# Optimization experiments

Hardware: AMD Instinct MI355X
Metric: run time of the kernel (lower is better)

## Reference

```python
import jax, jax.numpy as jnp
import numpy as np


def setup_inputs() -> dict:
    key = jax.random.key(0)
    ks = jax.random.split(key, 12)
    B, Nq, Ns, NODES = 128, 16, 256, 3
    V, E, C, H, OUT, NA = 50000, 300, 1024, 8, 300, 5000
    s = 0.05
    return {
        "he_ques": jax.random.randint(ks[0], (B, Nq, NODES), 0, V),
        "he_kg": jax.random.randint(ks[1], (B, Ns, NODES), 0, V),
        "emb": jax.random.normal(ks[2], (V, E), jnp.float32) * s,
        "q2h_w": jax.random.normal(ks[3], (C, E * NODES), jnp.float32) * s,
        "q2h_b": jax.random.normal(ks[4], (C,), jnp.float32) * s,
        "k2h_w": jax.random.normal(ks[5], (C, E * NODES), jnp.float32) * s,
        "k2h_b": jax.random.normal(ks[6], (C,), jnp.float32) * s,
        "h2att_w": jax.random.normal(ks[7], (H, C), jnp.float32) * s,
        "h2att_b": jax.random.normal(ks[8], (H,), jnp.float32) * s,
        "fc_w": jax.random.normal(ks[9], (OUT, C * H), jnp.float32) * s,
        "fc_b": jax.random.normal(ks[10], (OUT,), jnp.float32) * s,
        "glove_cands": jax.random.normal(ks[11], (NA, OUT), jnp.float32) * s,
    }


def reference(he_ques, he_kg, emb, q2h_w, q2h_b, k2h_w, k2h_b,
              h2att_w, h2att_b, fc_w, fc_b, glove_cands):
    B, Nq, _ = he_ques.shape
    Ns = he_kg.shape[1]
    H, C = h2att_w.shape
    # embed node indices and flatten per-hyperedge: [B, N, nodes*E]
    hq = emb[he_ques].reshape(B, Nq, -1)
    hs = emb[he_kg].reshape(B, Ns, -1)
    # linear projections (dropout p=0 in eval)
    hq = hq @ q2h_w.T + q2h_b  # [B, Nq, C]
    hs = hs @ k2h_w.T + k2h_b  # [B, Ns, C]
    # bilinear attention logits: h2att(outer(hq, hs)) fused into one einsum
    # logits[b,h,q,s] = sum_c hq[b,q,c] * hs[b,s,c] * W[h,c] + b[h]
    logits = jnp.einsum('bqc,bsc,hc->bhqs', hq, hs, h2att_w) + h2att_b[None, :, None, None]
    att = jax.nn.softmax(logits.reshape(B, H, Nq * Ns), axis=2).reshape(B, H, Nq, Ns)
    # per-head bilinear readout (replaces the per-head repeat+matmul loop):
    # out[b,h,c] = sum_{q,s} hq[b,q,c] * att[b,h,q,s] * hs[b,s,c]
    pooled = jnp.einsum('bqc,bhqs,bsc->bhc', hq, att, hs).reshape(B, H * C)
    out = pooled @ fc_w.T + fc_b  # [B, n_out]
    sim = out @ glove_cands.T  # [B, n_ans]
    return jax.nn.log_softmax(sim, axis=1)
```

## Files before the change

### kernel.cpp

```cpp
#include <hip/hip_runtime.h>
#include <stdint.h>


typedef short s16x8 __attribute__((ext_vector_type(8)));
typedef float f32x4 __attribute__((ext_vector_type(4)));

#define ASYNC_CP16(gsrc, ldst)                                                  \
  __builtin_amdgcn_global_load_lds(                                             \
      (const __attribute__((address_space(1))) void*)(gsrc),                    \
      (__attribute__((address_space(3))) void*)(ldst), 16, 0, 0)

__device__ __forceinline__ float bfr2f(uint16_t u) {
  return __builtin_bit_cast(float, (uint32_t)u << 16);
}
__device__ __forceinline__ uint16_t f2bfr(float f) {
  uint32_t u = __builtin_bit_cast(uint32_t, f);
  u += 0x7fffu + ((u >> 16) & 1u);
  return (uint16_t)(u >> 16);
}

__global__ __launch_bounds__(256) void cvt_all(
    const float* __restrict__ emb_f, const float* __restrict__ wk_f,
    const float* __restrict__ wq_f, const float* __restrict__ glove_f,
    const float* __restrict__ watt_f, const float* __restrict__ fc_f,
    uint16_t* __restrict__ EMB, uint16_t* __restrict__ WK,
    uint16_t* __restrict__ WQ, uint16_t* __restrict__ GLV,
    uint16_t* __restrict__ WATT, uint16_t* __restrict__ WFC) {
  const int idx = blockIdx.x * 256 + threadIdx.x;
  const int TOT1 = 61264 * 80;
  const int TOT2 = TOT1 + 1024;
  if (idx < TOT1) {
    const int row = idx / 80, j = idx % 80;
    const float* src;
    uint16_t* dst;
    int srow, svalid;
    if (row < 50000) {
      src = emb_f; dst = EMB; srow = row; svalid = 1;
    } else if (row < 53072) {
      src = wk_f; dst = WK; srow = row - 50000; svalid = 1;
    } else if (row < 56144) {
      src = wq_f; dst = WQ; srow = row - 53072; svalid = 1;
    } else {
      src = glove_f; dst = GLV; srow = row - 56144; svalid = (srow < 5000);
    }
    float4 v = make_float4(0.f, 0.f, 0.f, 0.f);
    if (svalid && j < 75) v = *(const float4*)(src + (size_t)srow * 300 + j * 4);
    ushort4 o;
    o.x = f2bfr(v.x); o.y = f2bfr(v.y); o.z = f2bfr(v.z); o.w = f2bfr(v.w);
    *(ushort4*)(dst + (size_t)srow * 320 + j * 4) = o;
  } else if (idx < TOT2) {
    const int i = idx - TOT1;
    float4 a = *(const float4*)(watt_f + i * 8);
    float4 b = *(const float4*)(watt_f + i * 8 + 4);
    ushort4 o0, o1;
    o0.x = f2bfr(a.x); o0.y = f2bfr(a.y); o0.z = f2bfr(a.z); o0.w = f2bfr(a.w);
    o1.x = f2bfr(b.x); o1.y = f2bfr(b.y); o1.z = f2bfr(b.z); o1.w = f2bfr(b.w);
    *(ushort4*)(WATT + i * 8) = o0;
    *(ushort4*)(WATT + i * 8 + 4) = o1;
  } else {
    const int i4 = idx - TOT2;
    if (i4 < 384 * 2048) {
      const int pos = i4 * 4;
      const int r = pos >> 13, c = pos & 8191;
      float4 v = make_float4(0.f, 0.f, 0.f, 0.f);
      if (r < 300) v = *(const float4*)(fc_f + (size_t)r * 8192 + c);
      ushort4 o;
      o.x = f2bfr(v.x); o.y = f2bfr(v.y); o.z = f2bfr(v.z); o.w = f2bfr(v.w);
      *(ushort4*)(WFC + (size_t)r * 8192 + c) = o;
    }
  }
}

__global__ __launch_bounds__(256) void gemm_gather2(
    const int* __restrict__ heK, const int* __restrict__ heQ,
    const uint16_t* __restrict__ emb,
    const uint16_t* __restrict__ WKp, const uint16_t* __restrict__ WQp,
    const float* __restrict__ bK, const float* __restrict__ bQ,
    uint16_t* __restrict__ HS, uint16_t* __restrict__ HQ) {
  __shared__ uint16_t ring[2 * 8192];
  __shared__ int sIdx[384];
  char* ringB = (char*)ring;

  const int t = threadIdx.x;
  const int lane = t & 63, wave = t >> 6;
  const int wr = wave >> 1, wc = wave & 1;
  const int fr = lane & 15, fq = lane >> 4;
  const int srow = t >> 2, skg = t & 3;
  const int skg2 = skg ^ ((srow >> 1) & 3);

  const int v = blockIdx.x + 8 * blockIdx.y;
  const int w = (v & 7) * 272 + (v >> 3);
  const int bx = w & 7, by = w >> 3;
  const int n0 = bx * 128;
  const bool isK = by < 256;
  const int m0 = (isK ? by : by - 256) * 128;
  const int* he = isK ? heK : heQ;
  const uint16_t* W = isK ? WKp : WQp;
  const float* bias = isK ? bK : bQ;
  uint16_t* C = isK ? HS : HQ;

  for (int i = t; i < 384; i += 256) sIdx[i] = he[(long)m0 * 3 + i];
  __syncthreads();

  uint32_t ea[2][3];
#pragma unroll
  for (int h = 0; h < 2; h++)
#pragma unroll
    for (int nd = 0; nd < 3; nd++)
      ea[h][nd] =
          (uint32_t)sIdx[(h * 64 + srow) * 3 + nd] * 640u + (uint32_t)(skg2 * 16);
  const uint16_t* Wr0 = W + (long)(n0 + srow) * 960 + skg2 * 8;
  const uint16_t* Wr1 = W + (long)(n0 + 64 + srow) * 960 + skg2 * 8;

  f32x4 zv = {0.f, 0.f, 0.f, 0.f};
  f32x4 acc[4][4];
#pragma unroll
  for (int i = 0; i < 4; i++)
#pragma unroll
    for (int j = 0; j < 4; j++) acc[i][j] = zv;

  int snd = 0, skk = 0, sk = 0, sbuf = 0;
  auto STAGE = [&]() {
    const int bb = sbuf * 16384;
    const uint32_t e0 = snd == 0 ? ea[0][0] : (snd == 1 ? ea[0][1] : ea[0][2]);
    const uint32_t e1 = snd == 0 ? ea[1][0] : (snd == 1 ? ea[1][1] : ea[1][2]);
    ASYNC_CP16((const char*)emb + e0 + skk * 64, ringB + bb + t * 16);
    ASYNC_CP16((const char*)emb + e1 + skk * 64, ringB + bb + 4096 + t * 16);
    ASYNC_CP16(Wr0 + sk, ringB + bb + 8192 + t * 16);
    ASYNC_CP16(Wr1 + sk, ringB + bb + 12288 + t * 16);
    sk += 32;
    if (++skk == 10) { skk = 0; ++snd; }
    sbuf ^= 1;
  };

  STAGE();

  const int fsw = (fq ^ ((fr >> 1) & 3)) * 8;
  int aof[4], bof[4];
#pragma unroll
  for (int mi = 0; mi < 4; mi++) aof[mi] = (wr * 64 + mi * 16 + fr) * 32 + fsw;
#pragma unroll
  for (int ni = 0; ni < 4; ni++)
    bof[ni] = 4096 + (wc * 64 + ni * 16 + fr) * 32 + fsw;

  int cbuf = 0;
  for (int kt = 0; kt < 30; ++kt) {
    if (kt < 29) {
      STAGE();
      asm volatile("s_waitcnt vmcnt(4)" ::: "memory");
    } else {
      asm volatile("s_waitcnt vmcnt(0)" ::: "memory");
    }
    __builtin_amdgcn_s_barrier();
    asm volatile("" ::: "memory");
    const uint16_t* base = ring + cbuf * 8192;
    s16x8 af[4], bv[4];
#pragma unroll
    for (int mi = 0; mi < 4; mi++) af[mi] = *(const s16x8*)(base + aof[mi]);
#pragma unroll
    for (int ni = 0; ni < 4; ni++) bv[ni] = *(const s16x8*)(base + bof[ni]);
    __builtin_amdgcn_s_setprio(1);
#pragma unroll
    for (int mi = 0; mi < 4; mi++)
#pragma unroll
      for (int ni = 0; ni < 4; ni++)
        acc[mi][ni] = __builtin_amdgcn_mfma_f32_16x16x32_bf16(
            af[mi], bv[ni], acc[mi][ni], 0, 0, 0);
    __builtin_amdgcn_s_setprio(0);
    asm volatile("s_waitcnt lgkmcnt(0)" ::: "memory");
    __builtin_amdgcn_s_barrier();
    cbuf ^= 1;
  }

#pragma unroll
  for (int ni = 0; ni < 4; ni++) {
    const int gn = n0 + wc * 64 + ni * 16 + fr;
    const float bval = bias[gn];
#pragma unroll
    for (int mi = 0; mi < 4; mi++) {
      const int gmb = m0 + wr * 64 + mi * 16 + fq * 4;
      uint16_t* cp = C + (long)gmb * 1024 + gn;
      cp[0]    = f2bfr(acc[mi][ni][0] + bval);
      cp[1024] = f2bfr(acc[mi][ni][1] + bval);
      cp[2048] = f2bfr(acc[mi][ni][2] + bval);
      cp[3072] = f2bfr(acc[mi][ni][3] + bval);
    }
  }
}

__global__ __launch_bounds__(256) void gemm_logits(
    const uint16_t* __restrict__ hq, const uint16_t* __restrict__ watt,
    const uint16_t* __restrict__ hs, uint16_t* __restrict__ att) {
  __shared__ uint16_t ring[3 * 4096];
  char* ringB = (char*)ring;

  const int t = threadIdx.x;
  const int lane = t & 63, wave = t >> 6;
  const int wr = wave >> 1, wc = wave & 1;
  const int fr = lane & 15, fq = lane >> 4;
  const int srow = t >> 2, skg = t & 3;
  const int skg2 = skg ^ ((srow >> 1) & 3);

  int bx = blockIdx.x, bz = blockIdx.z;
  {
    const int v = bx + 2 * bz;
    const int w = (v & 7) * 32 + (v >> 3);
    bx = w & 1;
    bz = w >> 1;
  }
  const int n0 = bx * 128;

  const uint16_t* Bs0 = hs + (long)bz * 262144 + (long)(n0 + srow) * 1024 + skg2 * 8;
  const uint16_t* Bs1 = hs + (long)bz * 262144 + (long)(n0 + 64 + srow) * 1024 + skg2 * 8;
  const uint16_t* hqp = hq + (long)(bz * 16 + fr) * 1024 + fq * 8;
  const uint16_t* wp0 = watt + (long)(wr * 4 + 0) * 1024 + fq * 8;
  const uint16_t* wp1 = watt + (long)(wr * 4 + 1) * 1024 + fq * 8;
  const uint16_t* wp2 = watt + (long)(wr * 4 + 2) * 1024 + fq * 8;
  const uint16_t* wp3 = watt + (long)(wr * 4 + 3) * 1024 + fq * 8;

  f32x4 zv = {0.f, 0.f, 0.f, 0.f};
  f32x4 acc[4][4];
#pragma unroll
  for (int i = 0; i < 4; i++)
#pragma unroll
    for (int j = 0; j < 4; j++) acc[i][j] = zv;

  int sbuf = 0, cbuf = 0;
  ASYNC_CP16(Bs0, ringB + t * 16);
  ASYNC_CP16(Bs1, ringB + 2048 + t * 16);
  ASYNC_CP16(Bs0 + 32, ringB + 4096 + t * 16);
  ASYNC_CP16(Bs1 + 32, ringB + 4096 + 2048 + t * 16);
  sbuf = 2;
  s16x8 hqA = *(const s16x8*)(hqp);
  s16x8 wA0 = *(const s16x8*)(wp0), wA1 = *(const s16x8*)(wp1);
  s16x8 wA2 = *(const s16x8*)(wp2), wA3 = *(const s16x8*)(wp3);
  s16x8 hqB, wB0, wB1, wB2, wB3;

  const int fsw = (fq ^ ((fr >> 1) & 3)) * 8;
  int bof[4];
#pragma unroll
  for (int ni = 0; ni < 4; ni++)
    bof[ni] = (wc * 64 + ni * 16 + fr) * 32 + fsw;

#define LOG_BODY(KT, HQS, W0S, W1S, W2S, W3S, HQD, W0D, W1D, W2D, W3D)          \
  {                                                                             \
    const int kt = (KT);                                                        \
    if (kt + 2 < 32) {                                                          \
      ASYNC_CP16(Bs0 + (kt + 2) * 32, ringB + sbuf * 4096 + t * 16);            \
      ASYNC_CP16(Bs1 + (kt + 2) * 32, ringB + sbuf * 4096 + 2048 + t * 16);     \
      if (++sbuf == 3) sbuf = 0;                                                \
    }                                                                           \
    if (kt + 1 < 32) {                                                          \
      const int ko = (kt + 1) * 32;                                             \
      HQD = *(const s16x8*)(hqp + ko);                                          \
      W0D = *(const s16x8*)(wp0 + ko); W1D = *(const s16x8*)(wp1 + ko);         \
      W2D = *(const s16x8*)(wp2 + ko); W3D = *(const s16x8*)(wp3 + ko);         \
    }                                                                           \
    asm volatile("s_waitcnt vmcnt(7)" ::: "memory");                            \
    __builtin_amdgcn_s_barrier();                                               \
    asm volatile("" ::: "memory");                                              \
    s16x8 af0, af1, af2, af3, bv[4];                                            \
    _Pragma("unroll") for (int j = 0; j < 8; j++) {                             \
      const float hv = bfr2f((uint16_t)HQS[j]);                                 \
      af0[j] = (short)f2bfr(hv * bfr2f((uint16_t)W0S[j]));                      \
      af1[j] = (short)f2bfr(hv * bfr2f((uint16_t)W1S[j]));                      \
      af2[j] = (short)f2bfr(hv * bfr2f((uint16_t)W2S[j]));                      \
      af3[j] = (short)f2bfr(hv * bfr2f((uint16_t)W3S[j]));                      \
    }                                                                           \
    const uint16_t* base = ring + cbuf * 4096;                                  \
    _Pragma("unroll") for (int ni = 0; ni < 4; ni++)                            \
        bv[ni] = *(const s16x8*)(base + bof[ni]);                               \
    __builtin_amdgcn_s_setprio(1);                                              \
    _Pragma("unroll") for (int ni = 0; ni < 4; ni++) {                          \
      acc[0][ni] = __builtin_amdgcn_mfma_f32_16x16x32_bf16(af0, bv[ni],         \
                                                           acc[0][ni], 0, 0, 0);\
      acc[1][ni] = __builtin_amdgcn_mfma_f32_16x16x32_bf16(af1, bv[ni],         \
                                                           acc[1][ni], 0, 0, 0);\
      acc[2][ni] = __builtin_amdgcn_mfma_f32_16x16x32_bf16(af2, bv[ni],         \
                                                           acc[2][ni], 0, 0, 0);\
      acc[3][ni] = __builtin_amdgcn_mfma_f32_16x16x32_bf16(af3, bv[ni],         \
                                                           acc[3][ni], 0, 0, 0);\
    }                                                                           \
    __builtin_amdgcn_s_setprio(0);                                              \
    asm volatile("s_waitcnt lgkmcnt(0)" ::: "memory");                          \
    __builtin_amdgcn_s_barrier();                                               \
    if (++cbuf == 3) cbuf = 0;                                                  \
  }

  for (int kt2 = 0; kt2 < 32; kt2 += 2) {
    LOG_BODY(kt2, hqA, wA0, wA1, wA2, wA3, hqB, wB0, wB1, wB2, wB3);
    LOG_BODY(kt2 + 1, hqB, wB0, wB1, wB2, wB3, hqA, wA0, wA1, wA2, wA3);
  }
#undef LOG_BODY

#pragma unroll
  for (int ni = 0; ni < 4; ni++) {
    const int gn = n0 + wc * 64 + ni * 16 + fr;
#pragma unroll
    for (int mi = 0; mi < 4; mi++)
#pragma unroll
      for (int j = 0; j < 4; j++) {
        const int gm = wr * 64 + mi * 16 + fq * 4 + j;
        att[(long)bz * 32768 + gm * 256 + gn] = f2bfr(acc[mi][ni][j]);
      }
  }
}

template <int SWZ>
__global__ __launch_bounds__(256) void gemm_pipe(
    const uint16_t* __restrict__ A, int lda, long sAb,
    const uint16_t* __restrict__ Bt, int ldb, long sBb,
    int ksteps, int kchunk,
    float* __restrict__ Cf, int ldcf, int nmax, long sCf) {
  __shared__ uint16_t ring[3 * 8192];
  char* ringB = (char*)ring;

  const int t = threadIdx.x;
  const int lane = t & 63, wave = t >> 6;
  const int wr = wave >> 1, wc = wave & 1;
  const int fr = lane & 15, fq = lane >> 4;
  const int srow = t >> 2, skg = t & 3;
  const int skg2 = skg ^ ((srow >> 1) & 3);

  int bx = blockIdx.x, bz = blockIdx.z;
  if (SWZ) {
    const int nwg = gridDim.x * gridDim.z;
    const int v = bx + gridDim.x * bz;
    const int w = (v & 7) * (nwg >> 3) + (v >> 3);
    bx = w % gridDim.x;
    bz = w / gridDim.x;
  }
  const int m0 = blockIdx.y * 128, n0 = bx * 128;
  const uint16_t* Ab = A + (long)bz * sAb;
  const uint16_t* Bb = Bt;

  f32x4 zv = {0.f, 0.f, 0.f, 0.f};
  f32x4 acc[4][4];
#pragma unroll
  for (int i = 0; i < 4; i++)
#pragma unroll
    for (int j = 0; j < 4; j++) acc[i][j] = zv;

  const long kbase = (long)bz * kchunk;
  const uint16_t* As0 = Ab + (long)(m0 + srow) * lda + kbase + skg2 * 8;
  const uint16_t* As1 = Ab + (long)(m0 + 64 + srow) * lda + kbase + skg2 * 8;
  const uint16_t* Bs0 = Bb + (long)(n0 + srow) * ldb + kbase + skg2 * 8;
  const uint16_t* Bs1 = Bb + (long)(n0 + 64 + srow) * ldb + kbase + skg2 * 8;

  int sk = 0, sbuf = 0;
  auto STAGE = [&]() {
    const int bb = sbuf * 16384;
    ASYNC_CP16(As0 + sk, ringB + bb + t * 16);
    ASYNC_CP16(As1 + sk, ringB + bb + 4096 + t * 16);
    ASYNC_CP16(Bs0 + sk, ringB + bb + 8192 + t * 16);
    ASYNC_CP16(Bs1 + sk, ringB + bb + 12288 + t * 16);
    sk += 32;
    if (++sbuf == 3) sbuf = 0;
  };

  STAGE();
  STAGE();

  const int fsw = (fq ^ ((fr >> 1) & 3)) * 8;
  int aof[4], bof[4];
#pragma unroll
  for (int mi = 0; mi < 4; mi++) aof[mi] = (wr * 64 + mi * 16 + fr) * 32 + fsw;
#pragma unroll
  for (int ni = 0; ni < 4; ni++)
    bof[ni] = 4096 + (wc * 64 + ni * 16 + fr) * 32 + fsw;

  int cbuf = 0;
  for (int kt = 0; kt < ksteps; ++kt) {
    if (kt + 2 < ksteps) STAGE();
    if (kt + 2 < ksteps)      asm volatile("s_waitcnt vmcnt(8)" ::: "memory");
    else if (kt + 1 < ksteps) asm volatile("s_waitcnt vmcnt(4)" ::: "memory");
    else                      asm volatile("s_waitcnt vmcnt(0)" ::: "memory");
    __builtin_amdgcn_s_barrier();
    asm volatile("" ::: "memory");
    const uint16_t* base = ring + cbuf * 8192;
    s16x8 af[4], bv[4];
#pragma unroll
    for (int mi = 0; mi < 4; mi++) af[mi] = *(const s16x8*)(base + aof[mi]);
#pragma unroll
    for (int ni = 0; ni < 4; ni++) bv[ni] = *(const s16x8*)(base + bof[ni]);
#pragma unroll
    for (int mi = 0; mi < 4; mi++)
#pragma unroll
      for (int ni = 0; ni < 4; ni++)
        acc[mi][ni] = __builtin_amdgcn_mfma_f32_16x16x32_bf16(
            af[mi], bv[ni], acc[mi][ni], 0, 0, 0);
    asm volatile("s_waitcnt lgkmcnt(0)" ::: "memory");
    __builtin_amdgcn_s_barrier();
    if (++cbuf == 3) cbuf = 0;
  }

#pragma unroll
  for (int ni = 0; ni < 4; ni++) {
    const int gn = n0 + wc * 64 + ni * 16 + fr;
    if (gn < nmax) {
#pragma unroll
      for (int mi = 0; mi < 4; mi++)
#pragma unroll
        for (int j = 0; j < 4; j++) {
          const int gm = m0 + wr * 64 + mi * 16 + fq * 4 + j;
          Cf[(long)bz * sCf + (long)gm * ldcf + gn] = acc[mi][ni][j];
        }
    }
  }
}

__global__ __launch_bounds__(256) void gemm_pv(
    const uint16_t* __restrict__ att, const uint16_t* __restrict__ hs,
    const uint16_t* __restrict__ hqp, uint16_t* __restrict__ pooled) {
  __shared__ uint16_t sT[128 * 264];
  __shared__ uint16_t sA[4096];
  __shared__ uint16_t sHq[2048];

  const int t = threadIdx.x;
  const int lane = t & 63, wave = t >> 6;
  const int wr = wave >> 1, wc = wave & 1;
  const int fr = lane & 15, fq = lane >> 4;
  const int srow = t >> 2, skg = t & 3;
  const int skg2 = skg ^ ((srow >> 1) & 3);

  int bx = blockIdx.x, bz = blockIdx.z;
  {
    const int v = bx + 8 * bz;
    const int w = (v & 7) * 128 + (v >> 3);
    bx = w & 7;
    bz = w >> 3;
  }
  const int n0 = bx * 128;

  const uint16_t* hsb = hs + (long)bz * 262144;
  const int sloc = t & 15, c8 = t >> 4;
  s16x8 vv[16];
#pragma unroll
  for (int p = 0; p < 16; p++)
    vv[p] = *(const s16x8*)(hsb + (long)(p * 16 + sloc) * 1024 + n0 + c8 * 8);
  *(s16x8*)(sHq + (t >> 4) * 128 + (t & 15) * 8) =
      *(const s16x8*)(hqp + (long)bz * 16384 + (long)(t >> 4) * 1024 + n0 +
                      (t & 15) * 8);
#pragma unroll
  for (int p = 0; p < 16; p++) {
    const int s = p * 16 + sloc;
#pragma unroll
    for (int j = 0; j < 8; j++)
      sT[(c8 * 8 + j) * 264 + s] = (uint16_t)vv[p][j];
  }
  __syncthreads();

  f32x4 zv = {0.f, 0.f, 0.f, 0.f};
  f32x4 acc[4][4];
#pragma unroll
  for (int i = 0; i < 4; i++)
#pragma unroll
    for (int j = 0; j < 4; j++) acc[i][j] = zv;

  const uint16_t* As0 = att + (long)bz * 32768 + (long)srow * 256 + skg2 * 8;
  const uint16_t* As1 = att + (long)bz * 32768 + (long)(64 + srow) * 256 + skg2 * 8;

  const int fsw = (fq ^ ((fr >> 1) & 3)) * 8;
  int aof[4];
#pragma unroll
  for (int mi = 0; mi < 4; mi++) aof[mi] = (wr * 64 + mi * 16 + fr) * 32 + fsw;

  for (int kt = 0; kt < 8; ++kt) {
    ASYNC_CP16(As0 + kt * 32, (char*)sA + t * 16);
    ASYNC_CP16(As1 + kt * 32, (char*)sA + 4096 + t * 16);
    __syncthreads();
    s16x8 af[4], bv[4];
#pragma unroll
    for (int mi = 0; mi < 4; mi++) af[mi] = *(const s16x8*)(sA + aof[mi]);
#pragma unroll
    for (int ni = 0; ni < 4; ni++)
      bv[ni] = *(const s16x8*)(sT + (wc * 64 + ni * 16 + fr) * 264 + kt * 32 +
                               fq * 8);
    __builtin_amdgcn_s_setprio(1);
#pragma unroll
    for (int mi = 0; mi < 4; mi++)
#pragma unroll
      for (int ni = 0; ni < 4; ni++)
        acc[mi][ni] = __builtin_amdgcn_mfma_f32_16x16x32_bf16(
            af[mi], bv[ni], acc[mi][ni], 0, 0, 0);
    __builtin_amdgcn_s_setprio(0);
    __syncthreads();
  }

#pragma unroll
  for (int mi = 0; mi < 4; mi++) {
    const int hh = wr * 4 + mi;
#pragma unroll
    for (int ni = 0; ni < 4; ni++) {
      const int col = wc * 64 + ni * 16 + fr;
      float p = 0.f;
#pragma unroll
      for (int j = 0; j < 4; j++)
        p += acc[mi][ni][j] * bfr2f(sHq[(fq * 4 + j) * 128 + col]);
      p += __shfl_xor(p, 16);
      p += __shfl_xor(p, 32);
      if (fq == 0)
        pooled[(long)bz * 8192 + hh * 1024 + n0 + col] = f2bfr(p);
    }
  }
}

__global__ __launch_bounds__(256) void softmax_att(uint16_t* __restrict__ att) {
  const int b = blockIdx.x >> 3, h = blockIdx.x & 7;
  uint16_t* base = att + (long)b * 32768 + h * 4096;
  const int t = threadIdx.x;
  __shared__ float red[8];
  s16x8 v0 = *(const s16x8*)(base + t * 16);
  s16x8 v1 = *(const s16x8*)(base + t * 16 + 8);
  float f[16];
#pragma unroll
  for (int j = 0; j < 8; j++) {
    f[j] = bfr2f((uint16_t)v0[j]);
    f[8 + j] = bfr2f((uint16_t)v1[j]);
  }
  float mx = f[0];
#pragma unroll
  for (int j = 1; j < 16; j++) mx = fmaxf(mx, f[j]);
#pragma unroll
  for (int d = 1; d < 64; d <<= 1) mx = fmaxf(mx, __shfl_xor(mx, d));
  if ((t & 63) == 0) red[t >> 6] = mx;
  __syncthreads();
  mx = fmaxf(fmaxf(red[0], red[1]), fmaxf(red[2], red[3]));
  float s = 0.f;
#pragma unroll
  for (int j = 0; j < 16; j++) {
    f[j] = __expf(f[j] - mx);
    s += f[j];
  }
#pragma unroll
  for (int d = 1; d < 64; d <<= 1) s += __shfl_xor(s, d);
  if ((t & 63) == 0) red[4 + (t >> 6)] = s;
  __syncthreads();
  const float ri = 1.f / (red[4] + red[5] + red[6] + red[7]);
  s16x8 o0, o1;
#pragma unroll
  for (int j = 0; j < 8; j++) {
    o0[j] = (short)f2bfr(f[j] * ri);
    o1[j] = (short)f2bfr(f[8 + j] * ri);
  }
  *(s16x8*)(base + t * 16) = o0;
  *(s16x8*)(base + t * 16 + 8) = o1;
}

__global__ __launch_bounds__(256) void cvt_out_k(const float* __restrict__ parts,
                                                 const float* __restrict__ fc_b,
                                                 uint16_t* __restrict__ outb) {
  int idx = blockIdx.x * 256 + threadIdx.x;
  if (idx >= 128 * 320) return;
  int m = idx / 320, n = idx % 320;
  float v = 0.f;
  if (n < 300) {
    v = fc_b[n];
#pragma unroll
    for (int ch = 0; ch < 32; ch++) v += parts[ch * 38400 + m * 300 + n];
  }
  outb[idx] = f2bfr(v);
}

__global__ __launch_bounds__(256) void logsoftmax_k(const float* __restrict__ sim,
                                                    float* __restrict__ out) {
  const int r = blockIdx.x, t = threadIdx.x;
  __shared__ float red[4];
  __shared__ float red2[4];
  const float* x = sim + (long)r * 5000;
  float mx = -1e30f;
  for (int i = t; i < 5000; i += 256) mx = fmaxf(mx, x[i]);
#pragma unroll
  for (int d = 1; d < 64; d <<= 1) mx = fmaxf(mx, __shfl_xor(mx, d));
  if ((t & 63) == 0) red[t >> 6] = mx;
  __syncthreads();
  mx = fmaxf(fmaxf(red[0], red[1]), fmaxf(red[2], red[3]));
  float s = 0.f;
  for (int i = t; i < 5000; i += 256) s += __expf(x[i] - mx);
#pragma unroll
  for (int d = 1; d < 64; d <<= 1) s += __shfl_xor(s, d);
  if ((t & 63) == 0) red2[t >> 6] = s;
  __syncthreads();
  s = red2[0] + red2[1] + red2[2] + red2[3];
  const float lse = mx + logf(s);
  float* o = out + (long)r * 5000;
  for (int i = t; i < 5000; i += 256) o[i] = x[i] - lse;
}

extern "C" void kernel_launch(void* const* d_in, const int* in_sizes, int n_in,
                              void* d_out, int out_size, void* d_ws, size_t ws_size,
                              hipStream_t stream) {
  (void)in_sizes; (void)n_in; (void)out_size; (void)ws_size;
  const int* he_q = (const int*)d_in[0];
  const int* he_k = (const int*)d_in[1];
  const float* emb_f = (const float*)d_in[2];
  const float* q2h_w = (const float*)d_in[3];
  const float* q2h_b = (const float*)d_in[4];
  const float* k2h_w = (const float*)d_in[5];
  const float* k2h_b = (const float*)d_in[6];
  const float* h2att_w = (const float*)d_in[7];
  const float* fc_w = (const float*)d_in[9];
  const float* fc_b = (const float*)d_in[10];
  const float* glove = (const float*)d_in[11];
  float* out = (float*)d_out;

  char* ws = (char*)d_ws;
  uint16_t* EMB   = (uint16_t*)(ws);
  uint16_t* WK    = (uint16_t*)(ws + 32000000);
  uint16_t* WQ    = (uint16_t*)(ws + 33966080);
  uint16_t* WATT  = (uint16_t*)(ws + 35932160);
  uint16_t* WFC   = (uint16_t*)(ws + 35948544);
  uint16_t* GLV   = (uint16_t*)(ws + 42240000);
  uint16_t* HQ    = (uint16_t*)(ws + 45516800);
  uint16_t* HS    = (uint16_t*)(ws + 49711104);
  uint16_t* ATT   = (uint16_t*)(ws + 183928832);
  uint16_t* POOL  = (uint16_t*)(ws + 192317440);
  uint16_t* OUTB  = (uint16_t*)(ws + 195643392);
  float*    SIM   = (float*)(ws + 195725312);
  float*    PARTS = (float*)(ws + 49711104);

  cvt_all<<<22221, 256, 0, stream>>>(emb_f, k2h_w, q2h_w, glove, h2att_w, fc_w,
                                     EMB, WK, WQ, GLV, WATT, WFC);

  gemm_gather2<<<dim3(8, 272), 256, 0, stream>>>(
      he_k, he_q, EMB, WK, WQ, k2h_b, q2h_b, HS, HQ);

  gemm_logits<<<dim3(2, 1, 128), 256, 0, stream>>>(HQ, WATT, HS, ATT);
  softmax_att<<<1024, 256, 0, stream>>>(ATT);

  gemm_pv<<<dim3(8, 1, 128), 256, 0, stream>>>(ATT, HS, HQ, POOL);

  gemm_pipe<0><<<dim3(3, 1, 32), 256, 0, stream>>>(
      POOL, 8192, 0, WFC, 8192, 0, 8, 256, PARTS, 300, 300, 38400);

  cvt_out_k<<<160, 256, 0, stream>>>(PARTS, fc_b, OUTB);

  gemm_pipe<0><<<dim3(40, 1, 1), 256, 0, stream>>>(
      OUTB, 320, 0, GLV, 320, 0, 10, 0, SIM, 5000, 5000, 0);

  logsoftmax_k<<<128, 256, 0, stream>>>(SIM, out);
}
```

Measured before the change: 193.7 us.

## Enlarge gather-GEMM tile to 256x256 with 8 waves and 4-stage pipeline

The fused embedding-gather projection GEMM moves from 128x128 tiles with 4 waves and double buffering to 256x256 tiles with 8 waves and a 4-deep async-copy ring in 128 KB of dynamic LDS. Each wave now computes 128x64 of the output, which raises MFMA work per LDS fragment load and cuts the global reloads of the gathered embeddings and weights. Index loads now come straight from global memory rather than going through shared memory. The costs are lower occupancy (one block per CU), more accumulator registers per wave, and only 544 blocks, which may leave the device unevenly loaded.

```diff
diff --git a/kernel.cpp b/kernel.cpp
--- a/kernel.cpp
+++ b/kernel.cpp
@@ -71,97 +71,100 @@
   }
 }
 
-__global__ __launch_bounds__(256) void gemm_gather2(
+__global__ __launch_bounds__(512) void gemm_gather8(
     const int* __restrict__ heK, const int* __restrict__ heQ,
     const uint16_t* __restrict__ emb,
     const uint16_t* __restrict__ WKp, const uint16_t* __restrict__ WQp,
     const float* __restrict__ bK, const float* __restrict__ bQ,
     uint16_t* __restrict__ HS, uint16_t* __restrict__ HQ) {
-  __shared__ uint16_t ring[2 * 8192];
-  __shared__ int sIdx[384];
+  extern __shared__ uint16_t ring[];
   char* ringB = (char*)ring;
 
   const int t = threadIdx.x;
   const int lane = t & 63, wave = t >> 6;
-  const int wr = wave >> 1, wc = wave & 1;
+  const int wr = wave >> 2, wcn = wave & 3;
   const int fr = lane & 15, fq = lane >> 4;
   const int srow = t >> 2, skg = t & 3;
   const int skg2 = skg ^ ((srow >> 1) & 3);
 
-  const int v = blockIdx.x + 8 * blockIdx.y;
-  const int w = (v & 7) * 272 + (v >> 3);
-  const int bx = w & 7, by = w >> 3;
-  const int n0 = bx * 128;
-  const bool isK = by < 256;
-  const int m0 = (isK ? by : by - 256) * 128;
+  const int v = blockIdx.x + 4 * blockIdx.y;
+  const int w = (v & 7) * 68 + (v >> 3);
+  const int bx = w & 3, by = w >> 2;
+  const int n0 = bx * 256;
+  const bool isK = by < 128;
+  const int m0g = (isK ? by : by - 128) * 256;
   const int* he = isK ? heK : heQ;
   const uint16_t* W = isK ? WKp : WQp;
   const float* bias = isK ? bK : bQ;
   uint16_t* C = isK ? HS : HQ;
 
-  for (int i = t; i < 384; i += 256) sIdx[i] = he[(long)m0 * 3 + i];
-  __syncthreads();
-
   uint32_t ea[2][3];
 #pragma unroll
   for (int h = 0; h < 2; h++)
 #pragma unroll
     for (int nd = 0; nd < 3; nd++)
-      ea[h][nd] =
-          (uint32_t)sIdx[(h * 64 + srow) * 3 + nd] * 640u + (uint32_t)(skg2 * 16);
+      ea[h][nd] = (uint32_t)he[(long)(m0g + h * 128 + srow) * 3 + nd] * 640u +
+                  (uint32_t)(skg2 * 16);
   const uint16_t* Wr0 = W + (long)(n0 + srow) * 960 + skg2 * 8;
-  const uint16_t* Wr1 = W + (long)(n0 + 64 + srow) * 960 + skg2 * 8;
+  const uint16_t* Wr1 = W + (long)(n0 + 128 + srow) * 960 + skg2 * 8;
+  const char* embB = (const char*)emb;
 
   f32x4 zv = {0.f, 0.f, 0.f, 0.f};
-  f32x4 acc[4][4];
-#pragma unroll
-  for (int i = 0; i < 4; i++)
+  f32x4 acc[8][4];
+#pragma unroll
+  for (int i = 0; i < 8; i++)
 #pragma unroll
     for (int j = 0; j < 4; j++) acc[i][j] = zv;
 
   int snd = 0, skk = 0, sk = 0, sbuf = 0;
   auto STAGE = [&]() {
-    const int bb = sbuf * 16384;
+    const int bb = sbuf * 32768;
     const uint32_t e0 = snd == 0 ? ea[0][0] : (snd == 1 ? ea[0][1] : ea[0][2]);
     const uint32_t e1 = snd == 0 ? ea[1][0] : (snd == 1 ? ea[1][1] : ea[1][2]);
-    ASYNC_CP16((const char*)emb + e0 + skk * 64, ringB + bb + t * 16);
-    ASYNC_CP16((const char*)emb + e1 + skk * 64, ringB + bb + 4096 + t * 16);
-    ASYNC_CP16(Wr0 + sk, ringB + bb + 8192 + t * 16);
-    ASYNC_CP16(Wr1 + sk, ringB + bb + 12288 + t * 16);
+    ASYNC_CP16(embB + e0 + skk * 64, ringB + bb + t * 16);
+    ASYNC_CP16(embB + e1 + skk * 64, ringB + bb + 8192 + t * 16);
+    ASYNC_CP16(Wr0 + sk, ringB + bb + 16384 + t * 16);
+    ASYNC_CP16(Wr1 + sk, ringB + bb + 24576 + t * 16);
     sk += 32;
     if (++skk == 10) { skk = 0; ++snd; }
-    sbuf ^= 1;
+    if (++sbuf == 4) sbuf = 0;
   };
 
   STAGE();
+  STAGE();
+  STAGE();
 
   const int fsw = (fq ^ ((fr >> 1) & 3)) * 8;
-  int aof[4], bof[4];
-#pragma unroll
-  for (int mi = 0; mi < 4; mi++) aof[mi] = (wr * 64 + mi * 16 + fr) * 32 + fsw;
+  int aof[8], bof[4];
+#pragma unroll
+  for (int mi = 0; mi < 8; mi++)
+    aof[mi] = (wr * 128 + mi * 16 + fr) * 32 + fsw;
 #pragma unroll
   for (int ni = 0; ni < 4; ni++)
-    bof[ni] = 4096 + (wc * 64 + ni * 16 + fr) * 32 + fsw;
-
-  int cbuf = 0;
-  for (int kt = 0; kt < 30; ++kt) {
-    if (kt < 29) {
+    bof[ni] = 8192 + (wcn * 64 + ni * 16 + fr) * 32 + fsw;
+
+  for (int s = 0; s < 30; ++s) {
+    if (s < 27) {
       STAGE();
+      asm volatile("s_waitcnt vmcnt(12)" ::: "memory");
+    } else if (s == 27) {
+      asm volatile("s_waitcnt vmcnt(8)" ::: "memory");
+    } else if (s == 28) {
       asm volatile("s_waitcnt vmcnt(4)" ::: "memory");
     } else {
       asm volatile("s_waitcnt vmcnt(0)" ::: "memory");
     }
     __builtin_amdgcn_s_barrier();
     asm volatile("" ::: "memory");
-    const uint16_t* base = ring + cbuf * 8192;
-    s16x8 af[4], bv[4];
-#pragma unroll
-    for (int mi = 0; mi < 4; mi++) af[mi] = *(const s16x8*)(base + aof[mi]);
+    const uint16_t* base = ring + (s & 3) * 16384;
+    s16x8 af[8], bv[4];
+#pragma unroll
+    for (int mi = 0; mi < 8; mi++) af[mi] = *(const s16x8*)(base + aof[mi]);
 #pragma unroll
     for (int ni = 0; ni < 4; ni++) bv[ni] = *(const s16x8*)(base + bof[ni]);
     __builtin_amdgcn_s_setprio(1);
 #pragma unroll
-    for (int mi = 0; mi < 4; mi++)
+    for (int mi = 0; mi < 8; mi++)
 #pragma unroll
       for (int ni = 0; ni < 4; ni++)
         acc[mi][ni] = __builtin_amdgcn_mfma_f32_16x16x32_bf16(
@@ -169,16 +172,15 @@
     __builtin_amdgcn_s_setprio(0);
     asm volatile("s_waitcnt lgkmcnt(0)" ::: "memory");
     __builtin_amdgcn_s_barrier();
-    cbuf ^= 1;
   }
 
 #pragma unroll
   for (int ni = 0; ni < 4; ni++) {
-    const int gn = n0 + wc * 64 + ni * 16 + fr;
+    const int gn = n0 + wcn * 64 + ni * 16 + fr;
     const float bval = bias[gn];
 #pragma unroll
-    for (int mi = 0; mi < 4; mi++) {
-      const int gmb = m0 + wr * 64 + mi * 16 + fq * 4;
+    for (int mi = 0; mi < 8; mi++) {
+      const int gmb = m0g + wr * 128 + mi * 16 + fq * 4;
       uint16_t* cp = C + (long)gmb * 1024 + gn;
       cp[0]    = f2bfr(acc[mi][ni][0] + bval);
       cp[1024] = f2bfr(acc[mi][ni][1] + bval);
@@ -619,10 +621,14 @@
   float*    SIM   = (float*)(ws + 195725312);
   float*    PARTS = (float*)(ws + 49711104);
 
+  (void)hipFuncSetAttribute(
+      reinterpret_cast<const void*>(gemm_gather8),
+      hipFuncAttributeMaxDynamicSharedMemorySize, 131072);
+
   cvt_all<<<22221, 256, 0, stream>>>(emb_f, k2h_w, q2h_w, glove, h2att_w, fc_w,
                                      EMB, WK, WQ, GLV, WATT, WFC);
 
-  gemm_gather2<<<dim3(8, 272), 256, 0, stream>>>(
+  gemm_gather8<<<dim3(4, 136), 512, 131072, stream>>>(
       he_k, he_q, EMB, WK, WQ, k2h_b, q2h_b, HS, HQ);
 
   gemm_logits<<<dim3(2, 1, 128), 256, 0, stream>>>(HQ, WATT, HS, ATT);
```

Result: slower. 226.6 us (+17.0%).
